# Performance work log

Hardware: AMD Instinct MI355X
Metric: run time of the kernel (lower is better)

## Reference

```python
import jax, jax.numpy as jnp
import numpy as np

N_DIMS = 64
N_HALF = N_DIMS // 2
HIDDEN = 512
N_LAYERS = 8
BATCH = 16384

IDX_EVEN = np.arange(0, N_DIMS, 2)  # mask != 0 for even layers
IDX_ODD = np.arange(1, N_DIMS, 2)


def _init_mlp_params(key, n_in, n_hidden, n_out, n_layers):
    ks = jax.random.split(key, 3)
    def lin(k, fi, fo):
        return jax.random.normal(k, (n_layers, fi, fo), dtype=jnp.float32) / np.sqrt(fi)
    W1 = lin(ks[0], n_in, n_hidden)
    W2 = lin(ks[1], n_hidden, n_hidden)
    W3 = lin(ks[2], n_hidden, n_out)
    b1 = jnp.zeros((n_layers, n_hidden), jnp.float32)
    b2 = jnp.zeros((n_layers, n_hidden), jnp.float32)
    b3 = jnp.zeros((n_layers, n_out), jnp.float32)
    return W1, b1, W2, b2, W3, b3


def setup_inputs() -> dict:
    key = jax.random.key(0)
    ky, kt, ks = jax.random.split(key, 3)
    y = jax.random.normal(ky, (BATCH, N_DIMS), dtype=jnp.float32)
    tW1, tb1, tW2, tb2, tW3, tb3 = _init_mlp_params(kt, N_HALF, HIDDEN, N_HALF, N_LAYERS)
    sW1, sb1, sW2, sb2, sW3, sb3 = _init_mlp_params(ks, N_HALF, HIDDEN, N_HALF, N_LAYERS)
    s_scale = jnp.ones((N_LAYERS, N_HALF), jnp.float32)
    s_shift = jnp.zeros((N_LAYERS, N_HALF), jnp.float32)
    return {
        "y": y,
        "tW1": tW1, "tb1": tb1, "tW2": tW2, "tb2": tb2, "tW3": tW3, "tb3": tb3,
        "sW1": sW1, "sb1": sb1, "sW2": sW2, "sb2": sb2, "sW3": sW3, "sb3": sb3,
        "s_scale": s_scale, "s_shift": s_shift,
    }


def _mlp(x, W1, b1, W2, b2, W3, b3):
    h = jax.nn.relu(x @ W1 + b1)
    h = jax.nn.relu(h @ W2 + b2)
    return h @ W3 + b3


def reference(y, tW1, tb1, tW2, tb2, tW3, tb3,
              sW1, sb1, sW2, sb2, sW3, sb3, s_scale, s_shift):
    z = y
    log_det = jnp.zeros_like(y)
    for i in range(N_LAYERS):
        i0 = IDX_EVEN if i % 2 == 0 else IDX_ODD  # transformed half
        i1 = IDX_ODD if i % 2 == 0 else IDX_EVEN  # conditioning half
        z0 = z[:, i0]  # [B, 32]
        z1 = z[:, i1]  # [B, 32]
        t = _mlp(z1, tW1[i], tb1[i], tW2[i], tb2[i], tW3[i], tb3[i])
        s = jnp.tanh(_mlp(z1, sW1[i], sb1[i], sW2[i], sb2[i], sW3[i], sb3[i])) * s_scale[i] + s_shift[i]
        z0 = z0 * jnp.exp(s) + t
        z = z.at[:, i0].set(z0)
        log_det = log_det.at[:, i0].add(s)
    return z, log_det
```

## Files before the change

### kernel.cpp

```cpp
#include <hip/hip_runtime.h>

typedef unsigned short u16;
typedef unsigned int   u32;
typedef _Float16 f16;
typedef __attribute__((ext_vector_type(8))) _Float16 half8;
typedef __attribute__((ext_vector_type(4))) float f32x4;

#define NBATCH 16384

__device__ __forceinline__ u16 f2h(float x) {
  union { f16 h; u16 u; } v; v.h = (f16)x; return v.u;
}

__global__ __launch_bounds__(256) void cvt_w(
    const float* __restrict__ tsrc, const float* __restrict__ ssrc,
    u16* __restrict__ dst, int M, int N)
{
  __shared__ float tile[32][33];
  int z = blockIdx.z;
  const float* src = ((z & 1) ? ssrc : tsrc) + (size_t)(z >> 1) * M * N;
  u16* d = dst + (size_t)z * M * N;
  int n0 = blockIdx.x * 32, m0 = blockIdx.y * 32;
  for (int r = 0; r < 4; r++) {
    int m = m0 + threadIdx.y + r * 8, n = n0 + threadIdx.x;
    tile[threadIdx.y + r * 8][threadIdx.x] = src[(size_t)m * N + n];
  }
  __syncthreads();
  for (int r = 0; r < 4; r++) {
    int n = n0 + threadIdx.y + r * 8, m = m0 + threadIdx.x;
    d[(size_t)n * M + m] = f2h(tile[threadIdx.x][threadIdx.y + r * 8]);
  }
}

__global__ __launch_bounds__(512, 2) void meganvp(
    const float* __restrict__ y,
    const u16* __restrict__ W1T, const u16* __restrict__ W2T, const u16* __restrict__ W3T,
    const float* __restrict__ tb1, const float* __restrict__ sb1,
    const float* __restrict__ tb2, const float* __restrict__ sb2,
    const float* __restrict__ tb3, const float* __restrict__ sb3,
    const float* __restrict__ s_scale, const float* __restrict__ s_shift,
    float* __restrict__ out)
{
  __shared__ u16 buf[64 * 512];
  __shared__ u16 X[64 * 40];
  __shared__ float TS[64 * 68];

  const int t = threadIdx.x;
  const int m0 = blockIdx.x * 64;
  const int lane = t & 63, w = t >> 6, lm = lane & 15, quad = lane >> 4;
  const int cw = w * 64;
  const int phase = blockIdx.x & 15;
  const int zr = t >> 3, zq = t & 7, c0 = zq * 8;

  float z[8], ld[8];
  {
    const float* yb = y + (size_t)(m0 + zr) * 64 + c0;
    f32x4 v0 = *(const f32x4*)&yb[0];
    f32x4 v1 = *(const f32x4*)&yb[4];
#pragma unroll
    for (int k = 0; k < 4; k++) { z[k] = v0[k]; z[4 + k] = v1[k]; }
#pragma unroll
    for (int e = 0; e < 8; e++) ld[e] = 0.f;
  }

  for (int layer = 0; layer < 8; layer++) {
    const int par = layer & 1;
    {
      union { u16 a[4]; uint2 v; } xv;
#pragma unroll
      for (int e = 0; e < 4; e++) xv.a[e] = f2h(z[2 * e + 1 - par]);
      *(uint2*)&X[zr * 40 + zq * 4] = xv.v;
    }
    __syncthreads();

    for (int net = 0; net < 2; net++) {
      const int idx = layer * 2 + net;

      {
        const float* b1p = (net ? sb1 : tb1) + layer * 512 + cw + lm;
        float bias1[4];
#pragma unroll
        for (int ct = 0; ct < 4; ct++) bias1[ct] = b1p[ct * 16];
        const u16* W1p = W1T + ((size_t)idx * 512 + cw + lm) * 32 + quad * 8;
        half8 bv[4];
#pragma unroll
        for (int ct = 0; ct < 4; ct++) bv[ct] = *(const half8*)&W1p[ct * 512];
        half8 av[4];
#pragma unroll
        for (int rt = 0; rt < 4; rt++)
          av[rt] = *(const half8*)&X[(rt * 16 + lm) * 40 + quad * 8];
        f32x4 zz = {0.f, 0.f, 0.f, 0.f};
        f32x4 acc[4][4];
#pragma unroll
        for (int rt = 0; rt < 4; rt++)
#pragma unroll
          for (int ct = 0; ct < 4; ct++)
            acc[rt][ct] = __builtin_amdgcn_mfma_f32_16x16x32_f16(av[rt], bv[ct], zz, 0, 0, 0);
#pragma unroll
        for (int rt = 0; rt < 4; rt++) {
          const int mrow = rt * 16 + quad * 4;
#pragma unroll
          for (int ct = 0; ct < 4; ct++) {
            const int n = cw + ct * 16 + lm;
#pragma unroll
            for (int r = 0; r < 4; r++) {
              float v = acc[rt][ct][r] + bias1[ct];
              v = v > 0.f ? v : 0.f;
              const int m = mrow + r;
              buf[m * 512 + ((((n >> 3) ^ (m & 7)) << 3) | (n & 7))] = f2h(v);
            }
          }
        }
      }
      __syncthreads();

      {
        const float* b2p = (net ? sb2 : tb2) + layer * 512 + cw + lm;
        float bias2[4];
#pragma unroll
        for (int ct = 0; ct < 4; ct++) bias2[ct] = b2p[ct * 16];
        const u16* W2p = W2T + ((size_t)idx * 512 + cw + lm) * 512 + quad * 8;
        f32x4 zz = {0.f, 0.f, 0.f, 0.f};
        f32x4 acc[4][4];
#pragma unroll
        for (int rt = 0; rt < 4; rt++)
#pragma unroll
          for (int ct = 0; ct < 4; ct++) acc[rt][ct] = zz;
        half8 bb[2][4];
        {
          const int kk0 = (phase & 15) * 32, kk1 = ((phase + 1) & 15) * 32;
#pragma unroll
          for (int ct = 0; ct < 4; ct++) {
            bb[0][ct] = *(const half8*)&W2p[ct * 8192 + kk0];
            bb[1][ct] = *(const half8*)&W2p[ct * 8192 + kk1];
          }
        }
#pragma unroll
        for (int ci = 0; ci < 16; ci++) {
          const int kk = ((ci + phase) & 15) * 32;
          half8 av[4];
#pragma unroll
          for (int rt = 0; rt < 4; rt++) {
            const int m = rt * 16 + lm;
            av[rt] = *(const half8*)&buf[m * 512 + ((((kk >> 3) + quad) ^ (m & 7)) << 3)];
          }
          half8 cur[4];
#pragma unroll
          for (int ct = 0; ct < 4; ct++) cur[ct] = bb[ci & 1][ct];
          if (ci < 14) {
            const int kn = ((ci + 2 + phase) & 15) * 32;
#pragma unroll
            for (int ct = 0; ct < 4; ct++)
              bb[ci & 1][ct] = *(const half8*)&W2p[ct * 8192 + kn];
          }
#pragma unroll
          for (int rt = 0; rt < 4; rt++)
#pragma unroll
            for (int ct = 0; ct < 4; ct++)
              acc[rt][ct] = __builtin_amdgcn_mfma_f32_16x16x32_f16(av[rt], cur[ct], acc[rt][ct], 0, 0, 0);
        }
        __syncthreads();
#pragma unroll
        for (int rt = 0; rt < 4; rt++) {
          const int mrow = rt * 16 + quad * 4;
#pragma unroll
          for (int ct = 0; ct < 4; ct++) {
            const int n = cw + ct * 16 + lm;
#pragma unroll
            for (int r = 0; r < 4; r++) {
              float v = acc[rt][ct][r] + bias2[ct];
              v = v > 0.f ? v : 0.f;
              const int m = mrow + r;
              buf[m * 512 + ((((n >> 3) ^ (m & 7)) << 3) | (n & 7))] = f2h(v);
            }
          }
        }
      }
      __syncthreads();

      {
        const int hr = (w & 3) * 16, hc = (w >> 2) * 16;
        const u16* W3p = W3T + ((size_t)idx * 32 + hc + lm) * 512 + quad * 8;
        f32x4 ha[2];
        ha[0] = (f32x4){0.f, 0.f, 0.f, 0.f}; ha[1] = ha[0];
        const int m = hr + lm;
#pragma unroll
        for (int ci = 0; ci < 16; ci++) {
          const int kk = ((ci + phase) & 15) * 32;
          half8 av = *(const half8*)&buf[m * 512 + ((((kk >> 3) + quad) ^ (m & 7)) << 3)];
          half8 bv = *(const half8*)&W3p[kk];
          ha[ci & 1] = __builtin_amdgcn_mfma_f32_16x16x32_f16(av, bv, ha[ci & 1], 0, 0, 0);
        }
        const int j = hc + lm;
        if (net == 0) {
          const float b3 = tb3[layer * 32 + j];
#pragma unroll
          for (int r = 0; r < 4; r++) {
            const int mm = hr + quad * 4 + r;
            TS[mm * 68 + 2 * j] = ha[0][r] + ha[1][r] + b3;
          }
        } else {
          const int jj = layer * 32 + j;
          const float b3 = sb3[jj], sc = s_scale[jj], sh = s_shift[jj];
#pragma unroll
          for (int r = 0; r < 4; r++) {
            const int mm = hr + quad * 4 + r;
            TS[mm * 68 + 2 * j + 1] = tanhf(ha[0][r] + ha[1][r] + b3) * sc + sh;
          }
        }
      }
      __syncthreads();
    }

    {
      const float* base = &TS[zr * 68 + zq * 8];
      f32x4 q0 = *(const f32x4*)&base[0];
      f32x4 q1 = *(const f32x4*)&base[4];
      float q[8];
#pragma unroll
      for (int k = 0; k < 4; k++) { q[k] = q0[k]; q[4 + k] = q1[k]; }
#pragma unroll
      for (int e = 0; e < 4; e++) {
        const float tv = q[2 * e], sv = q[2 * e + 1];
        const int zi = 2 * e + par;
        z[zi] = z[zi] * expf(sv) + tv;
        ld[zi] += sv;
      }
    }
    __syncthreads();
  }

  {
    float* zb = out + (size_t)(m0 + zr) * 64 + c0;
    float* lb = out + (size_t)NBATCH * 64 + (size_t)(m0 + zr) * 64 + c0;
    f32x4 v0, v1, l0, l1;
#pragma unroll
    for (int k = 0; k < 4; k++) {
      v0[k] = z[k]; v1[k] = z[4 + k];
      l0[k] = ld[k]; l1[k] = ld[4 + k];
    }
    *(f32x4*)&zb[0] = v0; *(f32x4*)&zb[4] = v1;
    *(f32x4*)&lb[0] = l0; *(f32x4*)&lb[4] = l1;
  }
}

extern "C" void kernel_launch(void* const* d_in, const int* in_sizes, int n_in,
                              void* d_out, int out_size, void* d_ws, size_t ws_size,
                              hipStream_t stream) {
  (void)in_sizes; (void)n_in; (void)out_size; (void)ws_size;
  const float* y   = (const float*)d_in[0];
  const float* tW1 = (const float*)d_in[1];
  const float* tb1 = (const float*)d_in[2];
  const float* tW2 = (const float*)d_in[3];
  const float* tb2 = (const float*)d_in[4];
  const float* tW3 = (const float*)d_in[5];
  const float* tb3 = (const float*)d_in[6];
  const float* sW1 = (const float*)d_in[7];
  const float* sb1 = (const float*)d_in[8];
  const float* sW2 = (const float*)d_in[9];
  const float* sb2 = (const float*)d_in[10];
  const float* sW3 = (const float*)d_in[11];
  const float* sb3 = (const float*)d_in[12];
  const float* s_scale = (const float*)d_in[13];
  const float* s_shift = (const float*)d_in[14];
  float* out = (float*)d_out;

  char* ws = (char*)d_ws;
  const size_t W1SZ = (size_t)16 * 512 * 32 * 2;
  const size_t W2SZ = (size_t)16 * 512 * 512 * 2;
  u16* W1 = (u16*)(ws);
  u16* W2 = (u16*)(ws + W1SZ);
  u16* W3 = (u16*)(ws + W1SZ + W2SZ);

  cvt_w<<<dim3(16, 1, 16), dim3(32, 8), 0, stream>>>(tW1, sW1, W1, 32, 512);
  cvt_w<<<dim3(16, 16, 16), dim3(32, 8), 0, stream>>>(tW2, sW2, W2, 512, 512);
  cvt_w<<<dim3(1, 16, 16), dim3(32, 8), 0, stream>>>(tW3, sW3, W3, 512, 32);

  meganvp<<<256, 512, 0, stream>>>(y, W1, W2, W3, tb1, sb1, tb2, sb2, tb3, sb3,
                                   s_scale, s_shift, out);
}
```

Baseline: 469.6 us.

## Merge weight conversions, double-buffer hidden LDS, deepen weight prefetch, drop barriers

```diff
diff --git a/kernel.cpp b/kernel.cpp
--- a/kernel.cpp
+++ b/kernel.cpp
@@ -12,15 +12,21 @@
   union { f16 h; u16 u; } v; v.h = (f16)x; return v.u;
 }
 
-__global__ __launch_bounds__(256) void cvt_w(
-    const float* __restrict__ tsrc, const float* __restrict__ ssrc,
-    u16* __restrict__ dst, int M, int N)
+__global__ __launch_bounds__(256) void cvt_all(
+    const float* __restrict__ tW1, const float* __restrict__ sW1,
+    const float* __restrict__ tW2, const float* __restrict__ sW2,
+    const float* __restrict__ tW3, const float* __restrict__ sW3,
+    u16* __restrict__ dW1, u16* __restrict__ dW2, u16* __restrict__ dW3)
 {
   __shared__ float tile[32][33];
-  int z = blockIdx.z;
+  const int z = blockIdx.z, bx = blockIdx.x;
+  const float *tsrc, *ssrc; u16* dst; int M, N, nt, mt;
+  if (bx < 16)       { tsrc = tW1; ssrc = sW1; dst = dW1; M = 32;  N = 512; nt = bx;           mt = 0; }
+  else if (bx < 272) { tsrc = tW2; ssrc = sW2; dst = dW2; M = 512; N = 512; nt = (bx - 16) & 15; mt = (bx - 16) >> 4; }
+  else               { tsrc = tW3; ssrc = sW3; dst = dW3; M = 512; N = 32;  nt = 0;            mt = bx - 272; }
   const float* src = ((z & 1) ? ssrc : tsrc) + (size_t)(z >> 1) * M * N;
   u16* d = dst + (size_t)z * M * N;
-  int n0 = blockIdx.x * 32, m0 = blockIdx.y * 32;
+  const int n0 = nt * 32, m0 = mt * 32;
   for (int r = 0; r < 4; r++) {
     int m = m0 + threadIdx.y + r * 8, n = n0 + threadIdx.x;
     tile[threadIdx.y + r * 8][threadIdx.x] = src[(size_t)m * N + n];
@@ -41,7 +47,8 @@
     const float* __restrict__ s_scale, const float* __restrict__ s_shift,
     float* __restrict__ out)
 {
-  __shared__ u16 buf[64 * 512];
+  __shared__ u16 bufA[64 * 512];
+  __shared__ u16 bufB[64 * 512];
   __shared__ u16 X[64 * 40];
   __shared__ float TS[64 * 68];
 
@@ -107,7 +114,7 @@
               float v = acc[rt][ct][r] + bias1[ct];
               v = v > 0.f ? v : 0.f;
               const int m = mrow + r;
-              buf[m * 512 + ((((n >> 3) ^ (m & 7)) << 3) | (n & 7))] = f2h(v);
+              bufA[m * 512 + ((((n >> 3) ^ (m & 7)) << 3) | (n & 7))] = f2h(v);
             }
           }
         }
@@ -126,14 +133,13 @@
         for (int rt = 0; rt < 4; rt++)
 #pragma unroll
           for (int ct = 0; ct < 4; ct++) acc[rt][ct] = zz;
-        half8 bb[2][4];
-        {
-          const int kk0 = (phase & 15) * 32, kk1 = ((phase + 1) & 15) * 32;
-#pragma unroll
-          for (int ct = 0; ct < 4; ct++) {
-            bb[0][ct] = *(const half8*)&W2p[ct * 8192 + kk0];
-            bb[1][ct] = *(const half8*)&W2p[ct * 8192 + kk1];
-          }
+        half8 bb[4][4];
+#pragma unroll
+        for (int p = 0; p < 4; p++) {
+          const int kp = ((p + phase) & 15) * 32;
+#pragma unroll
+          for (int ct = 0; ct < 4; ct++)
+            bb[p][ct] = *(const half8*)&W2p[ct * 8192 + kp];
         }
 #pragma unroll
         for (int ci = 0; ci < 16; ci++) {
@@ -142,24 +148,20 @@
 #pragma unroll
           for (int rt = 0; rt < 4; rt++) {
             const int m = rt * 16 + lm;
-            av[rt] = *(const half8*)&buf[m * 512 + ((((kk >> 3) + quad) ^ (m & 7)) << 3)];
-          }
-          half8 cur[4];
-#pragma unroll
-          for (int ct = 0; ct < 4; ct++) cur[ct] = bb[ci & 1][ct];
-          if (ci < 14) {
-            const int kn = ((ci + 2 + phase) & 15) * 32;
+            av[rt] = *(const half8*)&bufA[m * 512 + ((((kk >> 3) + quad) ^ (m & 7)) << 3)];
+          }
+#pragma unroll
+          for (int rt = 0; rt < 4; rt++)
 #pragma unroll
             for (int ct = 0; ct < 4; ct++)
-              bb[ci & 1][ct] = *(const half8*)&W2p[ct * 8192 + kn];
-          }
-#pragma unroll
-          for (int rt = 0; rt < 4; rt++)
+              acc[rt][ct] = __builtin_amdgcn_mfma_f32_16x16x32_f16(av[rt], bb[ci & 3][ct], acc[rt][ct], 0, 0, 0);
+          if (ci < 12) {
+            const int kn = ((ci + 4 + phase) & 15) * 32;
 #pragma unroll
             for (int ct = 0; ct < 4; ct++)
-              acc[rt][ct] = __builtin_amdgcn_mfma_f32_16x16x32_f16(av[rt], cur[ct], acc[rt][ct], 0, 0, 0);
-        }
-        __syncthreads();
+              bb[ci & 3][ct] = *(const half8*)&W2p[ct * 8192 + kn];
+          }
+        }
 #pragma unroll
         for (int rt = 0; rt < 4; rt++) {
           const int mrow = rt * 16 + quad * 4;
@@ -171,7 +173,7 @@
               float v = acc[rt][ct][r] + bias2[ct];
               v = v > 0.f ? v : 0.f;
               const int m = mrow + r;
-              buf[m * 512 + ((((n >> 3) ^ (m & 7)) << 3) | (n & 7))] = f2h(v);
+              bufB[m * 512 + ((((n >> 3) ^ (m & 7)) << 3) | (n & 7))] = f2h(v);
             }
           }
         }
@@ -184,12 +186,17 @@
         f32x4 ha[2];
         ha[0] = (f32x4){0.f, 0.f, 0.f, 0.f}; ha[1] = ha[0];
         const int m = hr + lm;
+        half8 pv[4];
+#pragma unroll
+        for (int p = 0; p < 4; p++)
+          pv[p] = *(const half8*)&W3p[((p + phase) & 15) * 32];
 #pragma unroll
         for (int ci = 0; ci < 16; ci++) {
           const int kk = ((ci + phase) & 15) * 32;
-          half8 av = *(const half8*)&buf[m * 512 + ((((kk >> 3) + quad) ^ (m & 7)) << 3)];
-          half8 bv = *(const half8*)&W3p[kk];
-          ha[ci & 1] = __builtin_amdgcn_mfma_f32_16x16x32_f16(av, bv, ha[ci & 1], 0, 0, 0);
+          half8 av = *(const half8*)&bufB[m * 512 + ((((kk >> 3) + quad) ^ (m & 7)) << 3)];
+          ha[ci & 1] = __builtin_amdgcn_mfma_f32_16x16x32_f16(av, pv[ci & 3], ha[ci & 1], 0, 0, 0);
+          if (ci < 12)
+            pv[ci & 3] = *(const half8*)&W3p[((ci + 4 + phase) & 15) * 32];
         }
         const int j = hc + lm;
         if (net == 0) {
@@ -227,7 +234,6 @@
         ld[zi] += sv;
       }
     }
-    __syncthreads();
   }
 
   {
@@ -272,9 +278,8 @@
   u16* W2 = (u16*)(ws + W1SZ);
   u16* W3 = (u16*)(ws + W1SZ + W2SZ);
 
-  cvt_w<<<dim3(16, 1, 16), dim3(32, 8), 0, stream>>>(tW1, sW1, W1, 32, 512);
-  cvt_w<<<dim3(16, 16, 16), dim3(32, 8), 0, stream>>>(tW2, sW2, W2, 512, 512);
-  cvt_w<<<dim3(1, 16, 16), dim3(32, 8), 0, stream>>>(tW3, sW3, W3, 512, 32);
+  cvt_all<<<dim3(288, 1, 16), dim3(32, 8), 0, stream>>>(tW1, sW1, tW2, sW2, tW3, sW3,
+                                                        W1, W2, W3);
 
   meganvp<<<256, 512, 0, stream>>>(y, W1, W2, W3, tb1, sb1, tb2, sb2, tb3, sb3,
                                    s_scale, s_shift, out);
```

Result: slower. 502.2 us (+6.9%).
